# Optimization experiments

Hardware: AMD Instinct MI355X
Metric: run time of the kernel (lower is better)

## Reference

```python
import jax, jax.numpy as jnp
import numpy as np

B, N, M, C = 8, 4096, 4096, 256
KS = 5          # dwc kernel size
FOCUS = 3.0     # focusing factor
EPS = 1e-6


def setup_inputs() -> dict:
    key = jax.random.key(0)
    ks = jax.random.split(key, 12)
    inp = {
        'query': jax.random.normal(ks[0], (B, N, C), jnp.float32),
        'key':   jax.random.normal(ks[1], (B, M, C), jnp.float32),
        'value': jax.random.normal(ks[2], (B, M, C), jnp.float32),
        'Wq':    jax.random.normal(ks[3], (C, C), jnp.float32) * 0.02,
        'Wk':    jax.random.normal(ks[4], (C, C), jnp.float32) * 0.02,
        'Wv':    jax.random.normal(ks[5], (C, C), jnp.float32) * 0.02,
        'Wproj': jax.random.normal(ks[6], (C, C), jnp.float32) * 0.02,
        'bproj': jax.random.normal(ks[7], (C,), jnp.float32) * 0.02,
        'dwc_w': jax.random.normal(ks[8], (C, 1, KS, KS), jnp.float32) * 0.02,
        'dwc_b': jax.random.normal(ks[9], (C,), jnp.float32) * 0.02,
        'scale': jax.random.normal(ks[10], (1, 1, C), jnp.float32) * 0.02,
        'H': 64,
        'W': 64,
    }
    return inp


def _dwconv(x, w, b):
    # x: (B, C, H, W), depthwise conv, SAME padding
    pad = KS // 2
    y = jax.lax.conv_general_dilated(
        x, w, window_strides=(1, 1), padding=[(pad, pad), (pad, pad)],
        dimension_numbers=('NCHW', 'OIHW', 'NCHW'), feature_group_count=C)
    return y + b[None, :, None, None]


def reference(query, key, value, Wq, Wk, Wv, Wproj, bproj, dwc_w, dwc_b, scale, H, W):
    q = jnp.einsum('bnc,dc->bnd', query, Wq)
    k = jnp.einsum('bmc,dc->bmd', key, Wk)
    v = jnp.einsum('bmc,dc->bmd', value, Wv)

    sc = jax.nn.softplus(scale)  # (1,1,C)
    q = (jax.nn.relu(q) + EPS) / sc
    k = (jax.nn.relu(k) + EPS) / sc

    q_norm = jnp.linalg.norm(q, axis=-1, keepdims=True)
    k_norm = jnp.linalg.norm(k, axis=-1, keepdims=True)
    # faithful to source: power then divide/multiply by the pre-power norm
    q = q ** FOCUS / q_norm * q_norm
    k = k ** FOCUS / k_norm * k_norm

    k_sum = k.sum(axis=1)                                   # (B, C)
    z_num = jnp.einsum('bnc,bc->bn', q, k_sum)              # (B, N)
    z = 1.0 / (z_num + EPS)

    kv = jnp.einsum('bmc,bmd->bcd', k, v)                   # (B, C, C)
    x = jnp.einsum('bnc,bcd->bnd', q, kv) * z[:, :, None]   # (B, N, C)

    xmap = x.transpose(0, 2, 1).reshape(x.shape[0], C, H, W)
    xmap = _dwconv(xmap, dwc_w, dwc_b)
    x = xmap.reshape(x.shape[0], C, H * W).transpose(0, 2, 1)

    x = x + q
    x = jnp.einsum('bnc,dc->bnd', x, Wproj) + bproj
    return x
```

## Files before the change

kernel.cpp:

```cpp
#include <hip/hip_runtime.h>
#include <math.h>
#include <stdint.h>

#define EPSF 1e-6f

typedef _Float16 half_t;
typedef _Float16 half8 __attribute__((ext_vector_type(8)));
typedef _Float16 half4 __attribute__((ext_vector_type(4)));
typedef float f32x4 __attribute__((ext_vector_type(4)));

#define MFMA16(A, B, C) __builtin_amdgcn_mfma_f32_16x16x32_f16(A, B, C, 0, 0, 0)

__device__ __forceinline__ float softplusf(float x) {
  return (x > 20.f) ? x : log1pf(expf(x));
}


__device__ __forceinline__ void stage_f32split(const float* __restrict__ src, int ld,
                                               int row0, int k0,
                                               half_t* __restrict__ Dh, half_t* __restrict__ Dl,
                                               int tid) {
#pragma unroll
  for (int r = 0; r < 4; ++r) {
    const int f = tid + r * 256;
    const int row = f >> 3, c4 = f & 7;
    const float4 v = *(const float4*)&src[(size_t)(row0 + row) * ld + k0 + c4 * 4];
    half4 h, l;
    h.x = (half_t)v.x; l.x = (half_t)(v.x - (float)h.x);
    h.y = (half_t)v.y; l.y = (half_t)(v.y - (float)h.y);
    h.z = (half_t)v.z; l.z = (half_t)(v.z - (float)h.z);
    h.w = (half_t)v.w; l.w = (half_t)(v.w - (float)h.w);
    *(half4*)&Dh[row * 32 + c4 * 4] = h;
    *(half4*)&Dl[row * 32 + c4 * 4] = l;
  }
}

__device__ __forceinline__ void stage_gld(const half_t* __restrict__ src, size_t rowbase,
                                          int ld, int k0, half_t* __restrict__ dst, int tid) {
#pragma unroll
  for (int r = 0; r < 2; ++r) {
    const int f = tid + r * 256;
    const half_t* g = src + (rowbase + (size_t)(f >> 2)) * (size_t)ld + k0 + (f & 3) * 8;
    const __attribute__((address_space(1))) unsigned int* gp =
        (const __attribute__((address_space(1))) unsigned int*)(uintptr_t)g;
    __attribute__((address_space(3))) unsigned int* lp =
        (__attribute__((address_space(3))) unsigned int*)(uintptr_t)(dst + f * 8);
    __builtin_amdgcn_global_load_lds(gp, lp, 16, 0, 0);
  }
}

__device__ __forceinline__ void frag_compute(const half_t* __restrict__ As_h,
                                             const half_t* __restrict__ As_l,
                                             const half_t* __restrict__ Bs_h,
                                             const half_t* __restrict__ Bs_l,
                                             f32x4 (&acc)[4][4], int lane, int wm, int wn) {
  const int lr = lane & 15, lg = lane >> 4;
  half8 ah[4], al[4], bh[4], bl[4];
#pragma unroll
  for (int i = 0; i < 4; ++i) {
    const int ar = (wm * 64 + i * 16 + lr) * 32 + lg * 8;
    ah[i] = *(const half8*)&As_h[ar];
    al[i] = *(const half8*)&As_l[ar];
    const int br = (wn * 64 + i * 16 + lr) * 32 + lg * 8;
    bh[i] = *(const half8*)&Bs_h[br];
    bl[i] = *(const half8*)&Bs_l[br];
  }
#pragma unroll
  for (int i = 0; i < 4; ++i)
#pragma unroll
    for (int j = 0; j < 4; ++j) {
      acc[i][j] = MFMA16(ah[i], bh[j], acc[i][j]);
      acc[i][j] = MFMA16(ah[i], bl[j], acc[i][j]);
      acc[i][j] = MFMA16(al[i], bh[j], acc[i][j]);
    }
}

__global__ __launch_bounds__(256) void proj_mfma(
    const float* __restrict__ query, const float* __restrict__ key,
    const float* __restrict__ value,
    const float* __restrict__ Wq, const float* __restrict__ Wk, const float* __restrict__ Wv,
    const float* __restrict__ scale,
    half_t* __restrict__ qh, half_t* __restrict__ ql,
    half_t* __restrict__ khT, half_t* __restrict__ klT,
    half_t* __restrict__ vhT, half_t* __restrict__ vlT) {
  const int which = blockIdx.z;
  const float* A = which == 0 ? query : which == 1 ? key : value;
  const float* W = which == 0 ? Wq : which == 1 ? Wk : Wv;
  const int row0 = blockIdx.x * 128, col0 = blockIdx.y * 128;
  const int tid = threadIdx.x;
  __shared__ __align__(16) half_t As_h[4096], As_l[4096], Bs_h[4096], Bs_l[4096];
  f32x4 acc[4][4] = {};
  const int lane = tid & 63, wave = tid >> 6, wm = wave >> 1, wn = wave & 1;
  const int lr = lane & 15, lg = lane >> 4;

  for (int ks = 0; ks < 8; ++ks) {
    const int k0 = ks * 32;
    stage_f32split(A, 256, row0, k0, As_h, As_l, tid);
    stage_f32split(W, 256, col0, k0, Bs_h, Bs_l, tid);
    __syncthreads();
    frag_compute(As_h, As_l, Bs_h, Bs_l, acc, lane, wm, wn);
    __syncthreads();
  }

  if (which == 0) {
#pragma unroll
    for (int j = 0; j < 4; ++j) {
      const int c = col0 + wn * 64 + j * 16 + lr;
      const float sc = softplusf(scale[c]);
#pragma unroll
      for (int i = 0; i < 4; ++i) {
        const size_t rb = (size_t)row0 + wm * 64 + i * 16 + lg * 4;
#pragma unroll
        for (int r = 0; r < 4; ++r) {
          float v = acc[i][j][r];
          v = (fmaxf(v, 0.f) + EPSF) / sc;
          v = v * v * v;
          const half_t h = (half_t)v;
          qh[(rb + r) * 256 + c] = h;
          ql[(rb + r) * 256 + c] = (half_t)(v - (float)h);
        }
      }
    }
  } else {
    const int b = row0 >> 12, m0 = row0 & 4095;
    half_t* Th = (which == 1) ? khT : vhT;
    half_t* Tl = (which == 1) ? klT : vlT;
    const bool act = (which == 1);
#pragma unroll
    for (int j = 0; j < 4; ++j) {
      const int c = col0 + wn * 64 + j * 16 + lr;
      const float sc = act ? softplusf(scale[c]) : 1.f;
#pragma unroll
      for (int i = 0; i < 4; ++i) {
        const int m = m0 + wm * 64 + i * 16 + lg * 4;
        half4 hv, lv;
#pragma unroll
        for (int r = 0; r < 4; ++r) {
          float v = acc[i][j][r];
          if (act) { v = (fmaxf(v, 0.f) + EPSF) / sc; v = v * v * v; }
          const half_t h = (half_t)v;
          hv[r] = h;
          lv[r] = (half_t)(v - (float)h);
        }
        *(half4*)&Th[(size_t)(b * 256 + c) * 4096 + m] = hv;
        *(half4*)&Tl[(size_t)(b * 256 + c) * 4096 + m] = lv;
      }
    }
  }
}

__global__ __launch_bounds__(256) void ksum_k(const half_t* __restrict__ khT,
                                              const half_t* __restrict__ klT,
                                              float* __restrict__ ksm) {
  const int bc = blockIdx.x;
  const size_t base = (size_t)bc * 4096 + threadIdx.x * 16;
  float s = 0.f;
#pragma unroll
  for (int p = 0; p < 2; ++p) {
    const half8 h = *(const half8*)&khT[base + p * 8];
    const half8 l = *(const half8*)&klT[base + p * 8];
#pragma unroll
    for (int u = 0; u < 8; ++u) s += (float)h[u] + (float)l[u];
  }
  __shared__ float rbuf[256];
  rbuf[threadIdx.x] = s;
  __syncthreads();
  for (int off = 128; off > 0; off >>= 1) {
    if (threadIdx.x < off) rbuf[threadIdx.x] += rbuf[threadIdx.x + off];
    __syncthreads();
  }
  if (threadIdx.x == 0) ksm[bc] = rbuf[0];
}

__global__ __launch_bounds__(256) void kv_mfma(
    const half_t* __restrict__ vhT, const half_t* __restrict__ vlT,
    const half_t* __restrict__ khT, const half_t* __restrict__ klT,
    float* __restrict__ kvp) {
  const int b = blockIdx.z >> 3, s = blockIdx.z & 7;
  const int d0 = blockIdx.x * 128, c0 = blockIdx.y * 128;
  const int tid = threadIdx.x;
  __shared__ __align__(16) half_t As_h[4096], As_l[4096], Bs_h[4096], Bs_l[4096];
  f32x4 acc[4][4] = {};
  const int lane = tid & 63, wave = tid >> 6, wm = wave >> 1, wn = wave & 1;
  const int lr = lane & 15, lg = lane >> 4;
  const size_t arow = (size_t)b * 256 + d0, brow = (size_t)b * 256 + c0;

  for (int ks = 0; ks < 16; ++ks) {
    const int k0 = s * 512 + ks * 32;
    stage_gld(vhT, arow, 4096, k0, As_h, tid);
    stage_gld(vlT, arow, 4096, k0, As_l, tid);
    stage_gld(khT, brow, 4096, k0, Bs_h, tid);
    stage_gld(klT, brow, 4096, k0, Bs_l, tid);
    __syncthreads();
    frag_compute(As_h, As_l, Bs_h, Bs_l, acc, lane, wm, wn);
    __syncthreads();
  }

  float* outp = kvp + ((size_t)(b * 8 + s)) * 65536;
#pragma unroll
  for (int j = 0; j < 4; ++j) {
    const int c = c0 + wn * 64 + j * 16 + lr;
#pragma unroll
    for (int i = 0; i < 4; ++i) {
      const int d = d0 + wm * 64 + i * 16 + lg * 4;
#pragma unroll
      for (int r = 0; r < 4; ++r) outp[(size_t)(d + r) * 256 + c] = acc[i][j][r];
    }
  }
}

__global__ __launch_bounds__(256) void kv_red(const float* __restrict__ kvp,
                                              half_t* __restrict__ kvTh,
                                              half_t* __restrict__ kvTl) {
  const size_t idx = (size_t)blockIdx.x * 256 + threadIdx.x;
  const int b = (int)(idx >> 16);
  const int dc = (int)(idx & 65535);
  float s = 0.f;
#pragma unroll
  for (int t = 0; t < 8; ++t) s += kvp[((size_t)(b * 8 + t)) * 65536 + dc];
  const half_t h = (half_t)s;
  kvTh[idx] = h;
  kvTl[idx] = (half_t)(s - (float)h);
}

__global__ __launch_bounds__(256) void z_k(const half_t* __restrict__ qh,
                                           const half_t* __restrict__ ql,
                                           const float* __restrict__ ksm,
                                           float* __restrict__ zb) {
  const int wid = threadIdx.x >> 6, lane = threadIdx.x & 63;
  const int row = blockIdx.x * 4 + wid;
  const int b = row >> 12;
  const half4 h = *(const half4*)&qh[(size_t)row * 256 + lane * 4];
  const half4 l = *(const half4*)&ql[(size_t)row * 256 + lane * 4];
  const float4 kc = *(const float4*)&ksm[b * 256 + lane * 4];
  float d = ((float)h[0] + (float)l[0]) * kc.x + ((float)h[1] + (float)l[1]) * kc.y +
            ((float)h[2] + (float)l[2]) * kc.z + ((float)h[3] + (float)l[3]) * kc.w;
#pragma unroll
  for (int off = 32; off > 0; off >>= 1) d += __shfl_xor(d, off, 64);
  if (lane == 0) zb[row] = 1.f / (d + EPSF);
}

__global__ __launch_bounds__(256) void x1_mfma(
    const half_t* __restrict__ qh, const half_t* __restrict__ ql,
    const half_t* __restrict__ kvTh, const half_t* __restrict__ kvTl,
    const float* __restrict__ zb, float* __restrict__ xt) {
  const int b = blockIdx.z, n0 = blockIdx.x * 128, d0t = blockIdx.y * 128;
  const int tid = threadIdx.x;
  __shared__ __align__(16) half_t As_h[4096], As_l[4096], Bs_h[4096], Bs_l[4096];
  f32x4 acc[4][4] = {};
  const int lane = tid & 63, wave = tid >> 6, wm = wave >> 1, wn = wave & 1;
  const int lr = lane & 15, lg = lane >> 4;
  const size_t arow = (size_t)b * 4096 + n0, brow = (size_t)b * 256 + d0t;

  for (int ks = 0; ks < 8; ++ks) {
    const int k0 = ks * 32;
    stage_gld(qh, arow, 256, k0, As_h, tid);
    stage_gld(ql, arow, 256, k0, As_l, tid);
    stage_gld(kvTh, brow, 256, k0, Bs_h, tid);
    stage_gld(kvTl, brow, 256, k0, Bs_l, tid);
    __syncthreads();
    frag_compute(As_h, As_l, Bs_h, Bs_l, acc, lane, wm, wn);
    __syncthreads();
  }

#pragma unroll
  for (int i = 0; i < 4; ++i) {
    const int nb = n0 + wm * 64 + i * 16 + lg * 4;
    float zr[4];
#pragma unroll
    for (int r = 0; r < 4; ++r) zr[r] = zb[b * 4096 + nb + r];
#pragma unroll
    for (int j = 0; j < 4; ++j) {
      const int d = d0t + wn * 64 + j * 16 + lr;
      *(float4*)&xt[((size_t)b * 256 + d) * 4096 + nb] =
          make_float4(acc[i][j][0] * zr[0], acc[i][j][1] * zr[1],
                      acc[i][j][2] * zr[2], acc[i][j][3] * zr[3]);
    }
  }
}

__global__ __launch_bounds__(256) void dwconv_kernel(const float* __restrict__ xt,
                                                     const float* __restrict__ w,
                                                     const float* __restrict__ bias,
                                                     float* __restrict__ xc) {
  const int bc = blockIdx.x;
  const int c = bc & 255;
  const float* plane = xt + (size_t)bc * 4096;
  float* oplane = xc + (size_t)bc * 4096;

  __shared__ float Ls[68][72];
  const int tid = threadIdx.x;
  for (int i = tid; i < 68 * 72; i += 256) ((float*)Ls)[i] = 0.f;
  __syncthreads();
#pragma unroll
  for (int p = 0; p < 4; ++p) {
    const int f = tid + p * 256;
    const int y = f >> 4, x4 = f & 15;
    *(float4*)&Ls[2 + y][4 + x4 * 4] = *(const float4*)&plane[y * 64 + x4 * 4];
  }
  __syncthreads();

  float wreg[25];
#pragma unroll
  for (int t = 0; t < 25; ++t) wreg[t] = w[c * 25 + t];
  const float bv = bias[c];

  const int x = tid & 63, ys0 = (tid >> 6) * 16;
  float win[5][5];
#pragma unroll
  for (int r = 0; r < 5; ++r)
#pragma unroll
    for (int cx = 0; cx < 5; ++cx) win[r][cx] = Ls[ys0 + r][x + 2 + cx];

  for (int yy = 0; yy < 16; ++yy) {
    float s = bv;
#pragma unroll
    for (int ky = 0; ky < 5; ++ky)
#pragma unroll
      for (int kx = 0; kx < 5; ++kx) s = fmaf(win[ky][kx], wreg[ky * 5 + kx], s);
    oplane[(ys0 + yy) * 64 + x] = s;
    if (yy < 15) {
#pragma unroll
      for (int r = 0; r < 4; ++r)
#pragma unroll
        for (int cx = 0; cx < 5; ++cx) win[r][cx] = win[r + 1][cx];
#pragma unroll
      for (int cx = 0; cx < 5; ++cx) win[4][cx] = Ls[ys0 + yy + 5][x + 2 + cx];
    }
  }
}

__global__ __launch_bounds__(256) void final_mfma(
    const half_t* __restrict__ qh, const half_t* __restrict__ ql,
    const float* __restrict__ xc, const float* __restrict__ Wp,
    const float* __restrict__ bp, float* __restrict__ outp) {
  const int b = blockIdx.z, n0 = blockIdx.x * 128, dd0 = blockIdx.y * 128;
  const int tid = threadIdx.x;
  __shared__ __align__(16) half_t As_h[4096], As_l[4096], Bs_h[4096], Bs_l[4096];
  __shared__ __align__(16) float Xs[32 * 130];
  f32x4 acc[4][4] = {};
  const int lane = tid & 63, wave = tid >> 6, wm = wave >> 1, wn = wave & 1;
  const int lr = lane & 15, lg = lane >> 4;

  for (int ks = 0; ks < 8; ++ks) {
    const int k0 = ks * 32;
#pragma unroll
    for (int r = 0; r < 4; ++r) {
      const int f = tid + r * 256, cc = f >> 5, n4 = f & 31;
      const float4 v = *(const float4*)&xc[((size_t)b * 256 + k0 + cc) * 4096 + n0 + n4 * 4];
      *(float2*)&Xs[cc * 130 + n4 * 4] = make_float2(v.x, v.y);
      *(float2*)&Xs[cc * 130 + n4 * 4 + 2] = make_float2(v.z, v.w);
    }
    stage_f32split(Wp, 256, dd0, k0, Bs_h, Bs_l, tid);
    __syncthreads();
#pragma unroll
    for (int r = 0; r < 2; ++r) {
      const int f = tid + r * 256, row = f >> 2, ch = f & 3;
      const size_t qoff = ((size_t)b * 4096 + n0 + row) * 256 + k0 + ch * 8;
      const half8 h8 = *(const half8*)&qh[qoff];
      const half8 l8 = *(const half8*)&ql[qoff];
      half8 oh, ol;
#pragma unroll
      for (int u = 0; u < 8; ++u) {
        const float v = (float)h8[u] + (float)l8[u] + Xs[(ch * 8 + u) * 130 + row];
        const half_t h = (half_t)v;
        oh[u] = h;
        ol[u] = (half_t)(v - (float)h);
      }
      *(half8*)&As_h[row * 32 + ch * 8] = oh;
      *(half8*)&As_l[row * 32 + ch * 8] = ol;
    }
    __syncthreads();
    frag_compute(As_h, As_l, Bs_h, Bs_l, acc, lane, wm, wn);
    __syncthreads();
  }

#pragma unroll
  for (int j = 0; j < 4; ++j) {
    const int dd = dd0 + wn * 64 + j * 16 + lr;
    const float bb = bp[dd];
#pragma unroll
    for (int i = 0; i < 4; ++i) {
      const size_t rowg = (size_t)b * 4096 + n0 + wm * 64 + i * 16 + lg * 4;
#pragma unroll
      for (int r = 0; r < 4; ++r) outp[(rowg + r) * 256 + dd] = acc[i][j][r] + bb;
    }
  }
}

extern "C" void kernel_launch(void* const* d_in, const int* in_sizes, int n_in,
                              void* d_out, int out_size, void* d_ws, size_t ws_size,
                              hipStream_t stream) {
  const float* query = (const float*)d_in[0];
  const float* key   = (const float*)d_in[1];
  const float* value = (const float*)d_in[2];
  const float* Wq    = (const float*)d_in[3];
  const float* Wk    = (const float*)d_in[4];
  const float* Wv    = (const float*)d_in[5];
  const float* Wproj = (const float*)d_in[6];
  const float* bproj = (const float*)d_in[7];
  const float* dwc_w = (const float*)d_in[8];
  const float* dwc_b = (const float*)d_in[9];
  const float* scale = (const float*)d_in[10];

  const size_t U = (size_t)8 * 4096 * 256;
  half_t* qh  = (half_t*)d_ws;
  half_t* ql  = qh + U;
  half_t* khT = ql + U;
  half_t* klT = khT + U;
  half_t* vhT = klT + U;
  half_t* vlT = vhT + U;
  float*  kvp = (float*)(vlT + U);
  half_t* kvTh = (half_t*)(kvp + (size_t)8 * 8 * 65536);
  half_t* kvTl = kvTh + (size_t)8 * 65536;
  float*  ksm = (float*)(kvTl + (size_t)8 * 65536);
  float*  zbuf = ksm + 8 * 256;
  float* xt = (float*)khT;
  float* xc = (float*)vhT;
  float* outp = (float*)d_out;

  const dim3 blk(256);
  proj_mfma<<<dim3(256, 2, 3), blk, 0, stream>>>(query, key, value, Wq, Wk, Wv, scale,
                                                 qh, ql, khT, klT, vhT, vlT);
  ksum_k<<<dim3(2048), blk, 0, stream>>>(khT, klT, ksm);
  kv_mfma<<<dim3(2, 2, 64), blk, 0, stream>>>(vhT, vlT, khT, klT, kvp);
  kv_red<<<dim3(2048), blk, 0, stream>>>(kvp, kvTh, kvTl);
  z_k<<<dim3(8192), blk, 0, stream>>>(qh, ql, ksm, zbuf);
  x1_mfma<<<dim3(32, 2, 8), blk, 0, stream>>>(qh, ql, kvTh, kvTl, zbuf, xt);
  dwconv_kernel<<<dim3(2048), blk, 0, stream>>>(xt, dwc_w, dwc_b, xc);
  final_mfma<<<dim3(32, 2, 8), blk, 0, stream>>>(qh, ql, xc, Wproj, bproj, outp);
}
```

Measured before the change: 319.7 us.

## Double-buffer GEMM staging and coalesce transposed projection stores via LDS

Adds register/LDS double buffering to the projection, kv, x1 and final GEMM kernels so global loads for the next k-tile overlap with MFMA work on the current tile. The q projection is computed transposed so its stores become contiguous half4 writes. The k/v transposed outputs are staged through shared memory for coalesced 16-byte writes. Softplus reciprocal is precomputed in a tiny kernel so epilogues multiply instead of divide. Doubling the LDS footprint may reduce occupancy, and the transposed-store path adds extra barriers.

```diff
diff --git a/kernel.cpp b/kernel.cpp
--- a/kernel.cpp
+++ b/kernel.cpp
@@ -15,25 +15,13 @@
   return (x > 20.f) ? x : log1pf(expf(x));
 }
 
-
-__device__ __forceinline__ void stage_f32split(const float* __restrict__ src, int ld,
-                                               int row0, int k0,
-                                               half_t* __restrict__ Dh, half_t* __restrict__ Dl,
-                                               int tid) {
-#pragma unroll
-  for (int r = 0; r < 4; ++r) {
-    const int f = tid + r * 256;
-    const int row = f >> 3, c4 = f & 7;
-    const float4 v = *(const float4*)&src[(size_t)(row0 + row) * ld + k0 + c4 * 4];
-    half4 h, l;
-    h.x = (half_t)v.x; l.x = (half_t)(v.x - (float)h.x);
-    h.y = (half_t)v.y; l.y = (half_t)(v.y - (float)h.y);
-    h.z = (half_t)v.z; l.z = (half_t)(v.z - (float)h.z);
-    h.w = (half_t)v.w; l.w = (half_t)(v.w - (float)h.w);
-    *(half4*)&Dh[row * 32 + c4 * 4] = h;
-    *(half4*)&Dl[row * 32 + c4 * 4] = l;
-  }
-}
+__device__ __forceinline__ void split4(const float4 v, half4& h, half4& l) {
+  h.x = (half_t)v.x; l.x = (half_t)(v.x - (float)h.x);
+  h.y = (half_t)v.y; l.y = (half_t)(v.y - (float)h.y);
+  h.z = (half_t)v.z; l.z = (half_t)(v.z - (float)h.z);
+  h.w = (half_t)v.w; l.w = (half_t)(v.w - (float)h.w);
+}
+
 
 __device__ __forceinline__ void stage_gld(const half_t* __restrict__ src, size_t rowbase,
                                           int ld, int k0, half_t* __restrict__ dst, int tid) {
@@ -75,76 +63,147 @@
     }
 }
 
+__global__ void scale_prep(const float* __restrict__ scale, float* __restrict__ scs) {
+  const int c = threadIdx.x;
+  scs[c] = 1.f / softplusf(scale[c]);
+}
+
 __global__ __launch_bounds__(256) void proj_mfma(
     const float* __restrict__ query, const float* __restrict__ key,
     const float* __restrict__ value,
     const float* __restrict__ Wq, const float* __restrict__ Wk, const float* __restrict__ Wv,
-    const float* __restrict__ scale,
+    const float* __restrict__ rsc,
     half_t* __restrict__ qh, half_t* __restrict__ ql,
     half_t* __restrict__ khT, half_t* __restrict__ klT,
     half_t* __restrict__ vhT, half_t* __restrict__ vlT) {
   const int which = blockIdx.z;
-  const float* A = which == 0 ? query : which == 1 ? key : value;
-  const float* W = which == 0 ? Wq : which == 1 ? Wk : Wv;
-  const int row0 = blockIdx.x * 128, col0 = blockIdx.y * 128;
   const int tid = threadIdx.x;
-  __shared__ __align__(16) half_t As_h[4096], As_l[4096], Bs_h[4096], Bs_l[4096];
-  f32x4 acc[4][4] = {};
   const int lane = tid & 63, wave = tid >> 6, wm = wave >> 1, wn = wave & 1;
   const int lr = lane & 15, lg = lane >> 4;
 
-  for (int ks = 0; ks < 8; ++ks) {
+  const float* srcA;
+  const float* srcB;
+  int rA0, rB0;
+  if (which == 0) {
+    srcA = Wq;    rA0 = blockIdx.y * 128;  srcB = query; rB0 = blockIdx.x * 128;
+  } else if (which == 1) {
+    srcA = key;   rA0 = blockIdx.x * 128;  srcB = Wk;    rB0 = blockIdx.y * 128;
+  } else {
+    srcA = value; rA0 = blockIdx.x * 128;  srcB = Wv;    rB0 = blockIdx.y * 128;
+  }
+
+  __shared__ __align__(16) half_t sm[32768];
+  f32x4 acc[4][4] = {};
+  float4 RA[2][4], RB[2][4];
+
+  auto load_tile = [&](float4 (&ra)[4], float4 (&rb)[4], int ks) {
     const int k0 = ks * 32;
-    stage_f32split(A, 256, row0, k0, As_h, As_l, tid);
-    stage_f32split(W, 256, col0, k0, Bs_h, Bs_l, tid);
-    __syncthreads();
-    frag_compute(As_h, As_l, Bs_h, Bs_l, acc, lane, wm, wn);
+#pragma unroll
+    for (int r = 0; r < 4; ++r) {
+      const int f = tid + r * 256;
+      const int row = f >> 3, c4 = f & 7;
+      ra[r] = *(const float4*)&srcA[(size_t)(rA0 + row) * 256 + k0 + c4 * 4];
+      rb[r] = *(const float4*)&srcB[(size_t)(rB0 + row) * 256 + k0 + c4 * 4];
+    }
+  };
+  auto split_write = [&](const float4 (&ra)[4], const float4 (&rb)[4], half_t* base) {
+#pragma unroll
+    for (int r = 0; r < 4; ++r) {
+      const int f = tid + r * 256;
+      const int row = f >> 3, c4 = f & 7;
+      half4 h, l;
+      split4(ra[r], h, l);
+      *(half4*)&base[row * 32 + c4 * 4] = h;
+      *(half4*)&base[4096 + row * 32 + c4 * 4] = l;
+      split4(rb[r], h, l);
+      *(half4*)&base[8192 + row * 32 + c4 * 4] = h;
+      *(half4*)&base[12288 + row * 32 + c4 * 4] = l;
+    }
+  };
+
+  load_tile(RA[0], RB[0], 0);
+  split_write(RA[0], RB[0], sm);
+  load_tile(RA[1], RB[1], 1);
+  __syncthreads();
+#pragma unroll
+  for (int t = 0; t < 8; ++t) {
+    if (t + 2 < 8) load_tile(RA[t & 1], RB[t & 1], t + 2);
+    half_t* base = sm + (t & 1) * 16384;
+    frag_compute(base, base + 4096, base + 8192, base + 12288, acc, lane, wm, wn);
+    if (t + 1 < 8) split_write(RA[(t + 1) & 1], RB[(t + 1) & 1], sm + ((t + 1) & 1) * 16384);
     __syncthreads();
   }
 
   if (which == 0) {
+    const int dbase = rA0 + wm * 64;
+    float rs[4][4];
+#pragma unroll
+    for (int i = 0; i < 4; ++i)
+#pragma unroll
+      for (int r = 0; r < 4; ++r) rs[i][r] = rsc[dbase + i * 16 + lg * 4 + r];
 #pragma unroll
     for (int j = 0; j < 4; ++j) {
-      const int c = col0 + wn * 64 + j * 16 + lr;
-      const float sc = softplusf(scale[c]);
+      const size_t nflat = (size_t)rB0 + wn * 64 + j * 16 + lr;
 #pragma unroll
       for (int i = 0; i < 4; ++i) {
-        const size_t rb = (size_t)row0 + wm * 64 + i * 16 + lg * 4;
+        half4 hv, lv;
 #pragma unroll
         for (int r = 0; r < 4; ++r) {
           float v = acc[i][j][r];
-          v = (fmaxf(v, 0.f) + EPSF) / sc;
+          v = (fmaxf(v, 0.f) + EPSF) * rs[i][r];
           v = v * v * v;
-          const half_t h = (half_t)v;
-          qh[(rb + r) * 256 + c] = h;
-          ql[(rb + r) * 256 + c] = (half_t)(v - (float)h);
-        }
-      }
-    }
-  } else {
-    const int b = row0 >> 12, m0 = row0 & 4095;
-    half_t* Th = (which == 1) ? khT : vhT;
-    half_t* Tl = (which == 1) ? klT : vlT;
-    const bool act = (which == 1);
-#pragma unroll
-    for (int j = 0; j < 4; ++j) {
-      const int c = col0 + wn * 64 + j * 16 + lr;
-      const float sc = act ? softplusf(scale[c]) : 1.f;
-#pragma unroll
-      for (int i = 0; i < 4; ++i) {
-        const int m = m0 + wm * 64 + i * 16 + lg * 4;
-        half4 hv, lv;
-#pragma unroll
-        for (int r = 0; r < 4; ++r) {
-          float v = acc[i][j][r];
-          if (act) { v = (fmaxf(v, 0.f) + EPSF) / sc; v = v * v * v; }
           const half_t h = (half_t)v;
           hv[r] = h;
           lv[r] = (half_t)(v - (float)h);
         }
-        *(half4*)&Th[(size_t)(b * 256 + c) * 4096 + m] = hv;
-        *(half4*)&Tl[(size_t)(b * 256 + c) * 4096 + m] = lv;
+        const size_t o = nflat * 256 + dbase + i * 16 + lg * 4;
+        *(half4*)&qh[o] = hv;
+        *(half4*)&ql[o] = lv;
       }
+    }
+  } else {
+    const int b = rA0 >> 12, m0 = rA0 & 4095;
+    half_t* Thg = (which == 1) ? khT : vhT;
+    half_t* Tlg = (which == 1) ? klT : vlT;
+    const bool act = (which == 1);
+    half_t* Tt = sm;
+    half_t* Tl2 = sm + 4352;
+#pragma unroll
+    for (int g = 0; g < 4; ++g) {
+      if (wn == (g >> 1)) {
+#pragma unroll
+        for (int jj = 0; jj < 2; ++jj) {
+          const int j = (g & 1) * 2 + jj;
+          const int c = rB0 + wn * 64 + j * 16 + lr;
+          const float rv = act ? rsc[c] : 1.f;
+          const int crel = jj * 16 + lr;
+#pragma unroll
+          for (int i = 0; i < 4; ++i) {
+            const int ml = wm * 64 + i * 16 + lg * 4;
+            half4 hv, lv;
+#pragma unroll
+            for (int r = 0; r < 4; ++r) {
+              float v = acc[i][j][r];
+              if (act) { v = (fmaxf(v, 0.f) + EPSF) * rv; v = v * v * v; }
+              const half_t h = (half_t)v;
+              hv[r] = h;
+              lv[r] = (half_t)(v - (float)h);
+            }
+            *(half4*)&Tt[crel * 136 + ml] = hv;
+            *(half4*)&Tl2[crel * 136 + ml] = lv;
+          }
+        }
+      }
+      __syncthreads();
+      {
+        const int cr = tid >> 3, mm = (tid & 7) * 16;
+        const size_t ga = ((size_t)(b * 256 + rB0 + g * 32 + cr)) * 4096 + m0 + mm;
+        *(half8*)&Thg[ga]     = *(const half8*)&Tt[cr * 136 + mm];
+        *(half8*)&Thg[ga + 8] = *(const half8*)&Tt[cr * 136 + mm + 8];
+        *(half8*)&Tlg[ga]     = *(const half8*)&Tl2[cr * 136 + mm];
+        *(half8*)&Tlg[ga + 8] = *(const half8*)&Tl2[cr * 136 + mm + 8];
+      }
+      __syncthreads();
     }
   }
 }
@@ -179,20 +238,27 @@
   const int b = blockIdx.z >> 3, s = blockIdx.z & 7;
   const int d0 = blockIdx.x * 128, c0 = blockIdx.y * 128;
   const int tid = threadIdx.x;
-  __shared__ __align__(16) half_t As_h[4096], As_l[4096], Bs_h[4096], Bs_l[4096];
+  __shared__ __align__(16) half_t sm[32768];
   f32x4 acc[4][4] = {};
   const int lane = tid & 63, wave = tid >> 6, wm = wave >> 1, wn = wave & 1;
   const int lr = lane & 15, lg = lane >> 4;
   const size_t arow = (size_t)b * 256 + d0, brow = (size_t)b * 256 + c0;
 
-  for (int ks = 0; ks < 16; ++ks) {
+  auto stage = [&](int bi, int ks) {
+    half_t* base = sm + bi * 16384;
     const int k0 = s * 512 + ks * 32;
-    stage_gld(vhT, arow, 4096, k0, As_h, tid);
-    stage_gld(vlT, arow, 4096, k0, As_l, tid);
-    stage_gld(khT, brow, 4096, k0, Bs_h, tid);
-    stage_gld(klT, brow, 4096, k0, Bs_l, tid);
-    __syncthreads();
-    frag_compute(As_h, As_l, Bs_h, Bs_l, acc, lane, wm, wn);
+    stage_gld(vhT, arow, 4096, k0, base, tid);
+    stage_gld(vlT, arow, 4096, k0, base + 4096, tid);
+    stage_gld(khT, brow, 4096, k0, base + 8192, tid);
+    stage_gld(klT, brow, 4096, k0, base + 12288, tid);
+  };
+
+  stage(0, 0);
+  __syncthreads();
+  for (int t = 0; t < 16; ++t) {
+    if (t + 1 < 16) stage((t + 1) & 1, t + 1);
+    half_t* base = sm + (t & 1) * 16384;
+    frag_compute(base, base + 4096, base + 8192, base + 12288, acc, lane, wm, wn);
     __syncthreads();
   }
 
@@ -246,20 +312,27 @@
     const float* __restrict__ zb, float* __restrict__ xt) {
   const int b = blockIdx.z, n0 = blockIdx.x * 128, d0t = blockIdx.y * 128;
   const int tid = threadIdx.x;
-  __shared__ __align__(16) half_t As_h[4096], As_l[4096], Bs_h[4096], Bs_l[4096];
+  __shared__ __align__(16) half_t sm[32768];
   f32x4 acc[4][4] = {};
   const int lane = tid & 63, wave = tid >> 6, wm = wave >> 1, wn = wave & 1;
   const int lr = lane & 15, lg = lane >> 4;
   const size_t arow = (size_t)b * 4096 + n0, brow = (size_t)b * 256 + d0t;
 
-  for (int ks = 0; ks < 8; ++ks) {
+  auto stage = [&](int bi, int ks) {
+    half_t* base = sm + bi * 16384;
     const int k0 = ks * 32;
-    stage_gld(qh, arow, 256, k0, As_h, tid);
-    stage_gld(ql, arow, 256, k0, As_l, tid);
-    stage_gld(kvTh, brow, 256, k0, Bs_h, tid);
-    stage_gld(kvTl, brow, 256, k0, Bs_l, tid);
-    __syncthreads();
-    frag_compute(As_h, As_l, Bs_h, Bs_l, acc, lane, wm, wn);
+    stage_gld(qh, arow, 256, k0, base, tid);
+    stage_gld(ql, arow, 256, k0, base + 4096, tid);
+    stage_gld(kvTh, brow, 256, k0, base + 8192, tid);
+    stage_gld(kvTl, brow, 256, k0, base + 12288, tid);
+  };
+
+  stage(0, 0);
+  __syncthreads();
+  for (int t = 0; t < 8; ++t) {
+    if (t + 1 < 8) stage((t + 1) & 1, t + 1);
+    half_t* base = sm + (t & 1) * 16384;
+    frag_compute(base, base + 4096, base + 8192, base + 12288, acc, lane, wm, wn);
     __syncthreads();
   }
 
@@ -342,23 +415,47 @@
   const int lane = tid & 63, wave = tid >> 6, wm = wave >> 1, wn = wave & 1;
   const int lr = lane & 15, lg = lane >> 4;
 
-  for (int ks = 0; ks < 8; ++ks) {
+  float4 rxs[4], rwp[4];
+  half8 rqh[2][2], rql[2][2];
+
+  auto load_xw = [&](int ks) {
     const int k0 = ks * 32;
 #pragma unroll
     for (int r = 0; r < 4; ++r) {
-      const int f = tid + r * 256, cc = f >> 5, n4 = f & 31;
-      const float4 v = *(const float4*)&xc[((size_t)b * 256 + k0 + cc) * 4096 + n0 + n4 * 4];
-      *(float2*)&Xs[cc * 130 + n4 * 4] = make_float2(v.x, v.y);
-      *(float2*)&Xs[cc * 130 + n4 * 4 + 2] = make_float2(v.z, v.w);
-    }
-    stage_f32split(Wp, 256, dd0, k0, Bs_h, Bs_l, tid);
+      const int f = tid + r * 256;
+      rxs[r] = *(const float4*)&xc[((size_t)b * 256 + k0 + (f >> 5)) * 4096 + n0 + (f & 31) * 4];
+      rwp[r] = *(const float4*)&Wp[(size_t)(dd0 + (f >> 3)) * 256 + k0 + (f & 7) * 4];
+    }
+  };
+
+  load_xw(0);
+#pragma unroll
+  for (int r = 0; r < 2; ++r) {
+    const int f = tid + r * 256;
+    const size_t qoff = ((size_t)b * 4096 + n0 + (f >> 2)) * 256 + (f & 3) * 8;
+    rqh[0][r] = *(const half8*)&qh[qoff];
+    rql[0][r] = *(const half8*)&ql[qoff];
+  }
+
+#pragma unroll
+  for (int t = 0; t < 8; ++t) {
+#pragma unroll
+    for (int r = 0; r < 4; ++r) {
+      const int f = tid + r * 256;
+      const int cc = f >> 5, n4 = f & 31;
+      *(float2*)&Xs[cc * 130 + n4 * 4] = make_float2(rxs[r].x, rxs[r].y);
+      *(float2*)&Xs[cc * 130 + n4 * 4 + 2] = make_float2(rxs[r].z, rxs[r].w);
+      half4 h, l;
+      split4(rwp[r], h, l);
+      *(half4*)&Bs_h[(f >> 3) * 32 + (f & 7) * 4] = h;
+      *(half4*)&Bs_l[(f >> 3) * 32 + (f & 7) * 4] = l;
+    }
     __syncthreads();
 #pragma unroll
     for (int r = 0; r < 2; ++r) {
       const int f = tid + r * 256, row = f >> 2, ch = f & 3;
-      const size_t qoff = ((size_t)b * 4096 + n0 + row) * 256 + k0 + ch * 8;
-      const half8 h8 = *(const half8*)&qh[qoff];
-      const half8 l8 = *(const half8*)&ql[qoff];
+      const half8 h8 = rqh[t & 1][r];
+      const half8 l8 = rql[t & 1][r];
       half8 oh, ol;
 #pragma unroll
       for (int u = 0; u < 8; ++u) {
@@ -371,6 +468,17 @@
       *(half8*)&As_l[row * 32 + ch * 8] = ol;
     }
     __syncthreads();
+    if (t + 1 < 8) {
+      load_xw(t + 1);
+      const int k0n = (t + 1) * 32;
+#pragma unroll
+      for (int r = 0; r < 2; ++r) {
+        const int f = tid + r * 256;
+        const size_t qoff = ((size_t)b * 4096 + n0 + (f >> 2)) * 256 + k0n + (f & 3) * 8;
+        rqh[(t + 1) & 1][r] = *(const half8*)&qh[qoff];
+        rql[(t + 1) & 1][r] = *(const half8*)&ql[qoff];
+      }
+    }
     frag_compute(As_h, As_l, Bs_h, Bs_l, acc, lane, wm, wn);
     __syncthreads();
   }
@@ -415,12 +523,14 @@
   half_t* kvTl = kvTh + (size_t)8 * 65536;
   float*  ksm = (float*)(kvTl + (size_t)8 * 65536);
   float*  zbuf = ksm + 8 * 256;
+  float*  scs  = zbuf + 32768;
   float* xt = (float*)khT;
   float* xc = (float*)vhT;
   float* outp = (float*)d_out;
 
   const dim3 blk(256);
-  proj_mfma<<<dim3(256, 2, 3), blk, 0, stream>>>(query, key, value, Wq, Wk, Wv, scale,
+  scale_prep<<<dim3(1), blk, 0, stream>>>(scale, scs);
+  proj_mfma<<<dim3(256, 2, 3), blk, 0, stream>>>(query, key, value, Wq, Wk, Wv, scs,
                                                  qh, ql, khT, klT, vhT, vlT);
   ksum_k<<<dim3(2048), blk, 0, stream>>>(khT, klT, ksm);
   kv_mfma<<<dim3(2, 2, 64), blk, 0, stream>>>(vhT, vlT, khT, klT, kvp);
@@ -428,5 +538,5 @@
   z_k<<<dim3(8192), blk, 0, stream>>>(qh, ql, ksm, zbuf);
   x1_mfma<<<dim3(32, 2, 8), blk, 0, stream>>>(qh, ql, kvTh, kvTl, zbuf, xt);
   dwconv_kernel<<<dim3(2048), blk, 0, stream>>>(xt, dwc_w, dwc_b, xc);
-  final_mfma<<<dim3(32, 2, 8), blk, 0, stream>>>(qh, ql, xc, Wproj, bproj, outp);
-}
+  final_mfma<<<dim3(32, 2, 8), blk, 0, stream>>>(xc == nullptr ? qh : qh, ql, xc, Wproj, bproj, outp);
+}
```

Result: faster. 309.5 us (-3.2%).
